# Optimization experiments

Hardware: AMD Instinct MI355X
Metric: run time of the kernel (lower is better)

## Reference

```python
import jax, jax.numpy as jnp
import numpy as np

N, D_IN, H, L, K, Q = 131072, 384, 256, 32, 512, 4


def _lin_init(key, fan_in, fan_out):
    s = 1.0 / np.sqrt(fan_in)
    kw, kb = jax.random.split(key)
    w = jax.random.uniform(kw, (fan_in, fan_out), minval=-s, maxval=s, dtype=jnp.float32)
    b = jax.random.uniform(kb, (fan_out,), minval=-s, maxval=s, dtype=jnp.float32)
    return w, b


def setup_inputs() -> dict:
    key = jax.random.key(0)
    ks = jax.random.split(key, 8)
    enc_w1, enc_b1 = _lin_init(ks[1], D_IN, H)
    enc_w2, enc_b2 = _lin_init(ks[2], H, H)
    enc_w3, enc_b3 = _lin_init(ks[3], H, L)
    dec_w1, dec_b1 = _lin_init(ks[4], L, H)
    dec_w2, dec_b2 = _lin_init(ks[5], H, H)
    dec_w3, dec_b3 = _lin_init(ks[6], H, D_IN)
    codebooks = jax.random.normal(ks[7], (Q, K, L), dtype=jnp.float32) * 0.02
    x = jax.random.normal(ks[0], (N, D_IN), dtype=jnp.float32)
    return dict(x=x,
                enc_w1=enc_w1, enc_b1=enc_b1, enc_w2=enc_w2, enc_b2=enc_b2,
                enc_w3=enc_w3, enc_b3=enc_b3,
                dec_w1=dec_w1, dec_b1=dec_b1, dec_w2=dec_w2, dec_b2=dec_b2,
                dec_w3=dec_w3, dec_b3=dec_b3,
                codebooks=codebooks)


def _encoder(x, w1, b1, w2, b2, w3, b3):
    h = jax.nn.relu(x @ w1 + b1)
    h = jax.nn.relu(h @ w2 + b2)
    return h @ w3 + b3


def _decoder(z, w1, b1, w2, b2, w3, b3):
    h = jax.nn.relu(z @ w1 + b1)
    h = jax.nn.relu(h @ w2 + b2)
    return h @ w3 + b3


def _residual_vq(z, codebooks):
    """Residual VQ: Q stages of nearest-codeword lookup on the running residual.
    Returns (z_quantized with straight-through, indices [N,Q], commitment loss)."""
    residual = z
    quant_sum = jnp.zeros_like(z)
    indices = []
    commit = jnp.float32(0.0)
    for q in range(codebooks.shape[0]):  # small fixed loop over quantizer stages
        cb = codebooks[q]  # [K, L]
        # squared L2 distances [N, K] via expansion (cdist + argmin)
        d = (jnp.sum(residual * residual, axis=-1, keepdims=True)
             - 2.0 * residual @ cb.T
             + jnp.sum(cb * cb, axis=-1))
        idx = jnp.argmin(d, axis=-1)          # [N]
        qv = cb[idx]                          # gather [N, L]
        commit = commit + jnp.mean((jax.lax.stop_gradient(qv) - residual) ** 2)
        quant_sum = quant_sum + qv
        residual = residual - jax.lax.stop_gradient(qv)
        indices.append(idx)
    # straight-through estimator
    z_q = z + jax.lax.stop_gradient(quant_sum - z)
    return z_q, jnp.stack(indices, axis=-1), commit


def reference(x, enc_w1, enc_b1, enc_w2, enc_b2, enc_w3, enc_b3,
              dec_w1, dec_b1, dec_w2, dec_b2, dec_w3, dec_b3, codebooks):
    z = _encoder(x, enc_w1, enc_b1, enc_w2, enc_b2, enc_w3, enc_b3)
    z_q, indices, commit = _residual_vq(z, codebooks)
    x_recon = _decoder(z_q, dec_w1, dec_b1, dec_w2, dec_b2, dec_w3, dec_b3)
    return x_recon, indices, commit
```

## Files before the change

kernel.cpp:

```cpp
#include <hip/hip_runtime.h>
#include <hip/hip_bf16.h>
#include <math.h>


#define N_ROWS 131072
#define D_IN   384
#define H_DIM  256
#define L_DIM  32
#define K_CB   512
#define Q_ST   4
#define VQ_RPB 256
#define NPART  (N_ROWS / VQ_RPB)

typedef __attribute__((ext_vector_type(8))) short short8v;
typedef __attribute__((ext_vector_type(4))) float f32x4;

__device__ __forceinline__ ushort f2bf(float v)
{
    __hip_bfloat16 b = __float2bfloat16(v);
    return *reinterpret_cast<ushort*>(&b);
}

__device__ __forceinline__ float np_sumsq32(const float* __restrict__ v)
{
    #pragma clang fp contract(off)
    float s0 = v[0]*v[0], s1 = v[1]*v[1], s2 = v[2]*v[2], s3 = v[3]*v[3];
    float s4 = v[4]*v[4], s5 = v[5]*v[5], s6 = v[6]*v[6], s7 = v[7]*v[7];
    s0 = s0 + v[8]*v[8];   s1 = s1 + v[9]*v[9];   s2 = s2 + v[10]*v[10]; s3 = s3 + v[11]*v[11];
    s4 = s4 + v[12]*v[12]; s5 = s5 + v[13]*v[13]; s6 = s6 + v[14]*v[14]; s7 = s7 + v[15]*v[15];
    s0 = s0 + v[16]*v[16]; s1 = s1 + v[17]*v[17]; s2 = s2 + v[18]*v[18]; s3 = s3 + v[19]*v[19];
    s4 = s4 + v[20]*v[20]; s5 = s5 + v[21]*v[21]; s6 = s6 + v[22]*v[22]; s7 = s7 + v[23]*v[23];
    s0 = s0 + v[24]*v[24]; s1 = s1 + v[25]*v[25]; s2 = s2 + v[26]*v[26]; s3 = s3 + v[27]*v[27];
    s4 = s4 + v[28]*v[28]; s5 = s5 + v[29]*v[29]; s6 = s6 + v[30]*v[30]; s7 = s7 + v[31]*v[31];
    return ((s0 + s1) + (s2 + s3)) + ((s4 + s5) + (s6 + s7));
}

template<bool RELU>
__global__ __launch_bounds__(256)
void gemm_bias(const float* __restrict__ A, const float* __restrict__ B,
               const float* __restrict__ bias, float* __restrict__ C,
               int K, int Nout)
{
    #pragma clang fp contract(off)
    __shared__ float As2[32][132];
    __shared__ float Bs[32][128];
    const int t  = threadIdx.x;
    const int tc = t & 15;
    const int tr = t >> 4;
    const size_t row0 = (size_t)blockIdx.x * 128;
    const int    col0 = blockIdx.y * 128;

    float acc[8][8];
    #pragma unroll
    for (int i = 0; i < 8; ++i)
        #pragma unroll
        for (int j = 0; j < 8; ++j) acc[i][j] = 0.f;

    const int ar = t >> 3, ak = (t & 7) << 2;
    const int br = t >> 5, bc = (t & 31) << 2;

    for (int k0 = 0; k0 < K; k0 += 32) {
        #pragma unroll
        for (int i = 0; i < 4; ++i) {
            int r = ar + (i << 5);
            float4 v = *reinterpret_cast<const float4*>(A + (row0 + r) * (size_t)K + k0 + ak);
            As2[ak + 0][r] = v.x; As2[ak + 1][r] = v.y;
            As2[ak + 2][r] = v.z; As2[ak + 3][r] = v.w;
        }
        #pragma unroll
        for (int i = 0; i < 4; ++i) {
            int r = br + (i << 3);
            float4 v = *reinterpret_cast<const float4*>(B + (size_t)(k0 + r) * Nout + col0 + bc);
            *reinterpret_cast<float4*>(&Bs[r][bc]) = v;
        }
        __syncthreads();
        #pragma unroll
        for (int k = 0; k < 32; ++k) {
            float a[8], b[8];
            *reinterpret_cast<float4*>(&a[0]) = *reinterpret_cast<const float4*>(&As2[k][tr << 3]);
            *reinterpret_cast<float4*>(&a[4]) = *reinterpret_cast<const float4*>(&As2[k][(tr << 3) + 4]);
            *reinterpret_cast<float4*>(&b[0]) = *reinterpret_cast<const float4*>(&Bs[k][tc << 2]);
            *reinterpret_cast<float4*>(&b[4]) = *reinterpret_cast<const float4*>(&Bs[k][(tc << 2) + 64]);
            #pragma unroll
            for (int i = 0; i < 8; ++i)
                #pragma unroll
                for (int j = 0; j < 8; ++j) acc[i][j] = fmaf(a[i], b[j], acc[i][j]);
        }
        __syncthreads();
    }

    #pragma unroll
    for (int i = 0; i < 8; ++i) {
        size_t r = row0 + (tr << 3) + i;
        int c1 = col0 + (tc << 2);
        int c2 = c1 + 64;
        float v1[4], v2[4];
        #pragma unroll
        for (int j = 0; j < 4; ++j) {
            float u1 = acc[i][j]     + bias[c1 + j];
            float u2 = acc[i][j + 4] + bias[c2 + j];
            if (RELU) { u1 = fmaxf(u1, 0.0f); u2 = fmaxf(u2, 0.0f); }
            v1[j] = u1; v2[j] = u2;
        }
        *reinterpret_cast<float4*>(C + r * Nout + c1) = *reinterpret_cast<float4*>(&v1[0]);
        *reinterpret_cast<float4*>(C + r * Nout + c2) = *reinterpret_cast<float4*>(&v2[0]);
    }
}

__global__ __launch_bounds__(256)
void gemm_z(const float* __restrict__ A, const float* __restrict__ W,
            const float* __restrict__ bv, float* __restrict__ Z)
{
    #pragma clang fp contract(off)
    __shared__ float As2[32][132];
    __shared__ float Ws[32][36];
    const int t = threadIdx.x;
    const int cgz = t & 7, rgz = t >> 3;
    const size_t row0 = (size_t)blockIdx.x * 128;

    float acc[4][4];
    #pragma unroll
    for (int i = 0; i < 4; ++i)
        #pragma unroll
        for (int j = 0; j < 4; ++j) acc[i][j] = 0.f;

    const int ar = t >> 3, ak = (t & 7) << 2;
    for (int k0 = 0; k0 < H_DIM; k0 += 32) {
        #pragma unroll
        for (int i = 0; i < 4; ++i) {
            int r = ar + (i << 5);
            float4 v = *reinterpret_cast<const float4*>(A + (row0 + r) * (size_t)H_DIM + k0 + ak);
            As2[ak + 0][r] = v.x; As2[ak + 1][r] = v.y;
            As2[ak + 2][r] = v.z; As2[ak + 3][r] = v.w;
        }
        {
            int kr = t >> 3, cc = (t & 7) << 2;
            float4 v = *reinterpret_cast<const float4*>(W + (size_t)(k0 + kr) * L_DIM + cc);
            *reinterpret_cast<float4*>(&Ws[kr][cc]) = v;
        }
        __syncthreads();
        #pragma unroll
        for (int k = 0; k < 32; ++k) {
            float a[4], w[4];
            *reinterpret_cast<float4*>(&a[0]) = *reinterpret_cast<const float4*>(&As2[k][rgz << 2]);
            *reinterpret_cast<float4*>(&w[0]) = *reinterpret_cast<const float4*>(&Ws[k][cgz << 2]);
            #pragma unroll
            for (int i = 0; i < 4; ++i)
                #pragma unroll
                for (int j = 0; j < 4; ++j) acc[i][j] = fmaf(a[i], w[j], acc[i][j]);
        }
        __syncthreads();
    }
    #pragma unroll
    for (int i = 0; i < 4; ++i) {
        size_t row = row0 + (rgz << 2) + i;
        float v[4];
        #pragma unroll
        for (int j = 0; j < 4; ++j) v[j] = acc[i][j] + bv[(cgz << 2) + j];
        *reinterpret_cast<float4*>(Z + row * L_DIM + (cgz << 2)) = *reinterpret_cast<float4*>(&v[0]);
    }
}

__global__ __launch_bounds__(256)
void cnorm_kernel(const float* __restrict__ cbs, float* __restrict__ cnorm)
{
    #pragma clang fp contract(off)
    int g = blockIdx.x * 256 + threadIdx.x;
    const float* c = cbs + (size_t)g * L_DIM;
    float cl[L_DIM];
    #pragma unroll
    for (int l = 0; l < L_DIM; ++l) cl[l] = c[l];
    cnorm[g] = np_sumsq32(cl);
}

__global__ __launch_bounds__(256)
void prep_wt(const float* __restrict__ W, ushort* __restrict__ Wt, int K, int N)
{
    int g = blockIdx.x * 256 + threadIdx.x;
    if (g >= K * N) return;
    int n = g / K, k = g - n * K;
    Wt[g] = f2bf(W[(size_t)k * N + n]);
}

__global__ __launch_bounds__(128)
void vq7_kernel(const float* __restrict__ zbuf, const float* __restrict__ cbs,
                const float* __restrict__ cnorm_g, ushort* __restrict__ zqb,
                float* __restrict__ idxOut, double* __restrict__ commitPart,
                int rowBase)
{
    #pragma clang fp contract(off)
    __shared__ float  cbL[K_CB * L_DIM];
    __shared__ float  cnL[K_CB];
    __shared__ double sred[128];

    const int t = threadIdx.x;
    const size_t lrow0 = (size_t)blockIdx.x * VQ_RPB + t;
    const size_t lrow1 = lrow0 + 128;
    const size_t grow0 = (size_t)rowBase + lrow0;
    const size_t grow1 = (size_t)rowBase + lrow1;

    float r0[L_DIM], r1[L_DIM];
    {
        const float4* zp0 = reinterpret_cast<const float4*>(zbuf + lrow0 * L_DIM);
        const float4* zp1 = reinterpret_cast<const float4*>(zbuf + lrow1 * L_DIM);
        #pragma unroll
        for (int j = 0; j < 8; ++j) {
            float4 a = zp0[j], b = zp1[j];
            r0[4*j+0]=a.x; r0[4*j+1]=a.y; r0[4*j+2]=a.z; r0[4*j+3]=a.w;
            r1[4*j+0]=b.x; r1[4*j+1]=b.y; r1[4*j+2]=b.z; r1[4*j+3]=b.w;
        }
    }

    int bidx0[Q_ST], bidx1[Q_ST];
    double cAcc = 0.0;

    #pragma unroll 1
    for (int q = 0; q < Q_ST; ++q) {
        __syncthreads();
        {
            const float4* src = reinterpret_cast<const float4*>(cbs + (size_t)q * K_CB * L_DIM);
            float4* dst = reinterpret_cast<float4*>(cbL);
            #pragma unroll
            for (int i = 0; i < 32; ++i) dst[t + (i << 7)] = src[t + (i << 7)];
            #pragma unroll
            for (int i = 0; i < 4; ++i)
                cnL[t + (i << 7)] = cnorm_g[q * K_CB + t + (i << 7)];
        }
        __syncthreads();

        float rr0 = np_sumsq32(r0);
        float rr1 = np_sumsq32(r1);
        float bd0 = __builtin_inff(), bd1 = __builtin_inff();
        int   bi0 = 0, bi1 = 0;

        #pragma unroll 1
        for (int c = 0; c < K_CB; c += 2) {
            const float4* w0 = reinterpret_cast<const float4*>(cbL + (c << 5));
            const float4* w1 = w0 + 8;
            float a00 = 0.f, a01 = 0.f, a10 = 0.f, a11 = 0.f;
            #pragma unroll
            for (int j = 0; j < 8; ++j) {
                float4 u = w0[j], v = w1[j];
                a00 = fmaf(r0[4*j+0], u.x, a00);  a01 = fmaf(r0[4*j+0], v.x, a01);
                a10 = fmaf(r1[4*j+0], u.x, a10);  a11 = fmaf(r1[4*j+0], v.x, a11);
                a00 = fmaf(r0[4*j+1], u.y, a00);  a01 = fmaf(r0[4*j+1], v.y, a01);
                a10 = fmaf(r1[4*j+1], u.y, a10);  a11 = fmaf(r1[4*j+1], v.y, a11);
                a00 = fmaf(r0[4*j+2], u.z, a00);  a01 = fmaf(r0[4*j+2], v.z, a01);
                a10 = fmaf(r1[4*j+2], u.z, a10);  a11 = fmaf(r1[4*j+2], v.z, a11);
                a00 = fmaf(r0[4*j+3], u.w, a00);  a01 = fmaf(r0[4*j+3], v.w, a01);
                a10 = fmaf(r1[4*j+3], u.w, a10);  a11 = fmaf(r1[4*j+3], v.w, a11);
            }
            float cn0 = cnL[c], cn1 = cnL[c + 1];
            float d00 = (rr0 - 2.0f * a00) + cn0;
            float d01 = (rr0 - 2.0f * a01) + cn1;
            float d10 = (rr1 - 2.0f * a10) + cn0;
            float d11 = (rr1 - 2.0f * a11) + cn1;
            if (d00 < bd0) { bd0 = d00; bi0 = c; }
            if (d01 < bd0) { bd0 = d01; bi0 = c + 1; }
            if (d10 < bd1) { bd1 = d10; bi1 = c; }
            if (d11 < bd1) { bd1 = d11; bi1 = c + 1; }
        }
        bidx0[q] = bi0;
        bidx1[q] = bi1;

        {
            const float4* p0 = reinterpret_cast<const float4*>(cbL + (bi0 << 5));
            const float4* p1 = reinterpret_cast<const float4*>(cbL + (bi1 << 5));
            float cs0 = 0.f, cs1 = 0.f;
            #pragma unroll
            for (int j = 0; j < 8; ++j) {
                float4 v0 = p0[j], v1 = p1[j];
                float df;
                df = v0.x - r0[4*j+0]; cs0 = fmaf(df, df, cs0); r0[4*j+0] = r0[4*j+0] - v0.x;
                df = v0.y - r0[4*j+1]; cs0 = fmaf(df, df, cs0); r0[4*j+1] = r0[4*j+1] - v0.y;
                df = v0.z - r0[4*j+2]; cs0 = fmaf(df, df, cs0); r0[4*j+2] = r0[4*j+2] - v0.z;
                df = v0.w - r0[4*j+3]; cs0 = fmaf(df, df, cs0); r0[4*j+3] = r0[4*j+3] - v0.w;
                df = v1.x - r1[4*j+0]; cs1 = fmaf(df, df, cs1); r1[4*j+0] = r1[4*j+0] - v1.x;
                df = v1.y - r1[4*j+1]; cs1 = fmaf(df, df, cs1); r1[4*j+1] = r1[4*j+1] - v1.y;
                df = v1.z - r1[4*j+2]; cs1 = fmaf(df, df, cs1); r1[4*j+2] = r1[4*j+2] - v1.z;
                df = v1.w - r1[4*j+3]; cs1 = fmaf(df, df, cs1); r1[4*j+3] = r1[4*j+3] - v1.w;
            }
            cAcc += (double)cs0;
            cAcc += (double)cs1;
        }
    }

    {
        float4 iv0 = make_float4((float)bidx0[0], (float)bidx0[1], (float)bidx0[2], (float)bidx0[3]);
        float4 iv1 = make_float4((float)bidx1[0], (float)bidx1[1], (float)bidx1[2], (float)bidx1[3]);
        *reinterpret_cast<float4*>(idxOut + grow0 * Q_ST) = iv0;
        *reinterpret_cast<float4*>(idxOut + grow1 * Q_ST) = iv1;
    }

    {
        const float4* zp0 = reinterpret_cast<const float4*>(zbuf + lrow0 * L_DIM);
        const float4* zp1 = reinterpret_cast<const float4*>(zbuf + lrow1 * L_DIM);
        ushort zq0[L_DIM], zq1[L_DIM];
        #pragma unroll
        for (int j = 0; j < 8; ++j) {
            float4 a = zp0[j], b = zp1[j];
            zq0[4*j+0] = f2bf(a.x - r0[4*j+0]);
            zq0[4*j+1] = f2bf(a.y - r0[4*j+1]);
            zq0[4*j+2] = f2bf(a.z - r0[4*j+2]);
            zq0[4*j+3] = f2bf(a.w - r0[4*j+3]);
            zq1[4*j+0] = f2bf(b.x - r1[4*j+0]);
            zq1[4*j+1] = f2bf(b.y - r1[4*j+1]);
            zq1[4*j+2] = f2bf(b.z - r1[4*j+2]);
            zq1[4*j+3] = f2bf(b.w - r1[4*j+3]);
        }
        uint4* o0 = reinterpret_cast<uint4*>(zqb + lrow0 * L_DIM);
        uint4* o1 = reinterpret_cast<uint4*>(zqb + lrow1 * L_DIM);
        const uint4* s0 = reinterpret_cast<const uint4*>(zq0);
        const uint4* s1 = reinterpret_cast<const uint4*>(zq1);
        #pragma unroll
        for (int j = 0; j < 4; ++j) { o0[j] = s0[j]; o1[j] = s1[j]; }
    }

    sred[t] = cAcc;
    __syncthreads();
    for (int s = 64; s > 0; s >>= 1) {
        if (t < s) sred[t] += sred[t + s];
        __syncthreads();
    }
    if (t == 0) commitPart[rowBase / VQ_RPB + blockIdx.x] = sred[0];
}

template<bool RELU, bool OUTBF16>
__global__ __launch_bounds__(256)
void mfma_gemm(const ushort* __restrict__ A, const ushort* __restrict__ Bt,
               const float* __restrict__ bias, void* __restrict__ Cout,
               int K, int Nout)
{
    __shared__ ushort As[128][40];
    __shared__ ushort Bs[128][40];
    const int t    = threadIdx.x;
    const int lane = t & 63;
    const int wid  = t >> 6;
    const int wr = wid >> 1, wc = wid & 1;
    const size_t row0 = (size_t)blockIdx.x * 128;
    const int    col0 = blockIdx.y * 128;

    f32x4 acc[4][4] = {};
    const int srow = t >> 1;
    const int sh   = (t & 1) << 4;

    for (int k0 = 0; k0 < K; k0 += 32) {
        {
            const ushort* ap = A + (row0 + srow) * (size_t)K + k0 + sh;
            uint4 v0 = *reinterpret_cast<const uint4*>(ap);
            uint4 v1 = *reinterpret_cast<const uint4*>(ap + 8);
            *reinterpret_cast<uint4*>(&As[srow][sh])     = v0;
            *reinterpret_cast<uint4*>(&As[srow][sh + 8]) = v1;
            const ushort* bp = Bt + (size_t)(col0 + srow) * K + k0 + sh;
            uint4 w0 = *reinterpret_cast<const uint4*>(bp);
            uint4 w1 = *reinterpret_cast<const uint4*>(bp + 8);
            *reinterpret_cast<uint4*>(&Bs[srow][sh])     = w0;
            *reinterpret_cast<uint4*>(&Bs[srow][sh + 8]) = w1;
        }
        __syncthreads();
        const int l15 = lane & 15, lk = (lane >> 4) << 3;
        short8v af[4], bf[4];
        #pragma unroll
        for (int f = 0; f < 4; ++f) {
            af[f] = *reinterpret_cast<const short8v*>(&As[(wr << 6) + (f << 4) + l15][lk]);
            bf[f] = *reinterpret_cast<const short8v*>(&Bs[(wc << 6) + (f << 4) + l15][lk]);
        }
        #pragma unroll
        for (int i = 0; i < 4; ++i)
            #pragma unroll
            for (int j = 0; j < 4; ++j)
                acc[i][j] = __builtin_amdgcn_mfma_f32_16x16x32_bf16(af[i], bf[j], acc[i][j], 0, 0, 0);
        __syncthreads();
    }

    const int l15 = lane & 15, lr4 = (lane >> 4) << 2;
    #pragma unroll
    for (int i = 0; i < 4; ++i) {
        #pragma unroll
        for (int j = 0; j < 4; ++j) {
            int col = col0 + (wc << 6) + (j << 4) + l15;
            float bv = bias[col];
            #pragma unroll
            for (int rj = 0; rj < 4; ++rj) {
                size_t row = row0 + (wr << 6) + (i << 4) + lr4 + rj;
                float v = acc[i][j][rj] + bv;
                if (RELU) v = fmaxf(v, 0.f);
                if (OUTBF16)
                    reinterpret_cast<ushort*>(Cout)[row * Nout + col] = f2bf(v);
                else
                    reinterpret_cast<float*>(Cout)[row * Nout + col] = v;
            }
        }
    }
}

__global__ __launch_bounds__(256)
void commit_finalize(const double* __restrict__ commitPart, float* __restrict__ outCommit)
{
    __shared__ double sred[256];
    const int t = threadIdx.x;
    double s = 0.0;
    for (int i = t; i < NPART; i += 256) s += commitPart[i];
    sred[t] = s;
    __syncthreads();
    for (int st = 128; st > 0; st >>= 1) {
        if (t < st) sred[t] += sred[t + st];
        __syncthreads();
    }
    if (t == 0)
        outCommit[0] = (float)(sred[0] / ((double)N_ROWS * (double)L_DIM));
}

extern "C" void kernel_launch(void* const* d_in, const int* in_sizes, int n_in,
                              void* d_out, int out_size, void* d_ws, size_t ws_size,
                              hipStream_t stream)
{
    const float* x      = (const float*)d_in[0];
    const float* enc_w1 = (const float*)d_in[1];
    const float* enc_b1 = (const float*)d_in[2];
    const float* enc_w2 = (const float*)d_in[3];
    const float* enc_b2 = (const float*)d_in[4];
    const float* enc_w3 = (const float*)d_in[5];
    const float* enc_b3 = (const float*)d_in[6];
    const float* dec_w1 = (const float*)d_in[7];
    const float* dec_b1 = (const float*)d_in[8];
    const float* dec_w2 = (const float*)d_in[9];
    const float* dec_b2 = (const float*)d_in[10];
    const float* dec_w3 = (const float*)d_in[11];
    const float* dec_b3 = (const float*)d_in[12];
    const float* cbs    = (const float*)d_in[13];

    float* out       = (float*)d_out;
    float* xrec      = out;
    float* idxOut    = out + (size_t)N_ROWS * D_IN;
    float* commitOut = idxOut + (size_t)N_ROWS * Q_ST;

    char*   wsb        = (char*)d_ws;
    float*  cnorm      = (float*)wsb;
    double* commitPart = (double*)(wsb + 8192);
    ushort* w1t        = (ushort*)(wsb + 12288);
    ushort* w2t        = (ushort*)(wsb + 28672);
    ushort* w3t        = (ushort*)(wsb + 159744);
    char*   bufs       = wsb + 360448;

    size_t availB = (ws_size > 360448) ? ws_size - 360448 : 0;
    long long chunk = (long long)(availB / 3264);
    chunk = (chunk / 256) * 256;
    if (chunk > N_ROWS) chunk = N_ROWS;
    if (chunk < 256) chunk = 256;

    float*  zbuf = (float*)bufs;
    float*  bufA = zbuf + (size_t)chunk * L_DIM;
    float*  bufB = bufA + (size_t)chunk * H_DIM;
    ushort* zqb  = (ushort*)(bufB + (size_t)chunk * H_DIM);
    ushort* h1b  = zqb + (size_t)chunk * L_DIM;
    ushort* h2b  = h1b + (size_t)chunk * H_DIM;

    cnorm_kernel<<<8, 256, 0, stream>>>(cbs, cnorm);
    prep_wt<<<(L_DIM  * H_DIM + 255) / 256, 256, 0, stream>>>(dec_w1, w1t, L_DIM, H_DIM);
    prep_wt<<<(H_DIM * H_DIM + 255) / 256, 256, 0, stream>>>(dec_w2, w2t, H_DIM, H_DIM);
    prep_wt<<<(H_DIM * D_IN + 255) / 256, 256, 0, stream>>>(dec_w3, w3t, H_DIM, D_IN);

    for (long long ro = 0; ro < N_ROWS; ro += chunk) {
        long long R = N_ROWS - ro;
        if (R > chunk) R = chunk;
        dim3 g2((unsigned)(R / 128), 2);
        dim3 g3((unsigned)(R / 128), 3);
        gemm_bias<true><<<g2, 256, 0, stream>>>(x + ro * D_IN, enc_w1, enc_b1, bufA, D_IN, H_DIM);
        gemm_bias<true><<<g2, 256, 0, stream>>>(bufA, enc_w2, enc_b2, bufB, H_DIM, H_DIM);
        gemm_z<<<(unsigned)(R / 128), 256, 0, stream>>>(bufB, enc_w3, enc_b3, zbuf);
        vq7_kernel<<<(unsigned)(R / VQ_RPB), 128, 0, stream>>>(zbuf, cbs, cnorm, zqb,
                                                               idxOut, commitPart, (int)ro);
        mfma_gemm<true,  true ><<<g2, 256, 0, stream>>>(zqb, w1t, dec_b1, h1b, L_DIM, H_DIM);
        mfma_gemm<true,  true ><<<g2, 256, 0, stream>>>(h1b, w2t, dec_b2, h2b, H_DIM, H_DIM);
        mfma_gemm<false, false><<<g3, 256, 0, stream>>>(h2b, w3t, dec_b3, xrec + ro * D_IN, H_DIM, D_IN);
    }

    commit_finalize<<<1, 256, 0, stream>>>(commitPart, commitOut);
}
```

Baseline: 1.068 ms.

## Split VQ codeword search across four waves with shared-memory argmin merge

The VQ kernel now runs 256 threads per block over 128 rows. Each of the four wavefronts scans a quarter of the 512 codewords for the same 64 row pairs, and the per-wave minima are merged through shared memory with lowest-index tie-breaking. This cuts the serial per-thread codeword loop by four and doubles the block count, aiming at better latency hiding and occupancy in the distance search. In exchange it adds an extra barrier and shared-memory merge per stage, repeats the residual update in every wave, and moves the workspace offsets so the larger commit-partial array fits.

New measurement: 932.4 us. 1.15x faster.

```diff
diff --git a/kernel.cpp b/kernel.cpp
--- a/kernel.cpp
+++ b/kernel.cpp
@@ -9,7 +9,7 @@
 #define L_DIM  32
 #define K_CB   512
 #define Q_ST   4
-#define VQ_RPB 256
+#define VQ_RPB 128
 #define NPART  (N_ROWS / VQ_RPB)
 
 typedef __attribute__((ext_vector_type(8))) short short8v;
@@ -182,8 +182,8 @@
     Wt[g] = f2bf(W[(size_t)k * N + n]);
 }
 
-__global__ __launch_bounds__(128)
-void vq7_kernel(const float* __restrict__ zbuf, const float* __restrict__ cbs,
+__global__ __launch_bounds__(256)
+void vq9_kernel(const float* __restrict__ zbuf, const float* __restrict__ cbs,
                 const float* __restrict__ cnorm_g, ushort* __restrict__ zqb,
                 float* __restrict__ idxOut, double* __restrict__ commitPart,
                 int rowBase)
@@ -191,13 +191,18 @@
     #pragma clang fp contract(off)
     __shared__ float  cbL[K_CB * L_DIM];
     __shared__ float  cnL[K_CB];
-    __shared__ double sred[128];
+    __shared__ float  sd0[4][64], sd1[4][64];
+    __shared__ int    si0[4][64], si1[4][64];
+    __shared__ double sred[256];
 
     const int t = threadIdx.x;
-    const size_t lrow0 = (size_t)blockIdx.x * VQ_RPB + t;
-    const size_t lrow1 = lrow0 + 128;
+    const int w = t >> 6;
+    const int l = t & 63;
+    const size_t lrow0 = (size_t)blockIdx.x * VQ_RPB + l;
+    const size_t lrow1 = lrow0 + 64;
     const size_t grow0 = (size_t)rowBase + lrow0;
     const size_t grow1 = (size_t)rowBase + lrow1;
+    const int c0 = w << 7;
 
     float r0[L_DIM], r1[L_DIM];
     {
@@ -221,20 +226,20 @@
             const float4* src = reinterpret_cast<const float4*>(cbs + (size_t)q * K_CB * L_DIM);
             float4* dst = reinterpret_cast<float4*>(cbL);
             #pragma unroll
-            for (int i = 0; i < 32; ++i) dst[t + (i << 7)] = src[t + (i << 7)];
-            #pragma unroll
-            for (int i = 0; i < 4; ++i)
-                cnL[t + (i << 7)] = cnorm_g[q * K_CB + t + (i << 7)];
+            for (int i = 0; i < 16; ++i) dst[t + (i << 8)] = src[t + (i << 8)];
+            cnL[t]       = cnorm_g[q * K_CB + t];
+            cnL[t + 256] = cnorm_g[q * K_CB + t + 256];
         }
         __syncthreads();
 
         float rr0 = np_sumsq32(r0);
         float rr1 = np_sumsq32(r1);
         float bd0 = __builtin_inff(), bd1 = __builtin_inff();
-        int   bi0 = 0, bi1 = 0;
+        int   bi0 = c0, bi1 = c0;
 
         #pragma unroll 1
-        for (int c = 0; c < K_CB; c += 2) {
+        for (int cc = 0; cc < 128; cc += 2) {
+            const int c = c0 + cc;
             const float4* w0 = reinterpret_cast<const float4*>(cbL + (c << 5));
             const float4* w1 = w0 + 8;
             float a00 = 0.f, a01 = 0.f, a10 = 0.f, a11 = 0.f;
@@ -260,12 +265,26 @@
             if (d10 < bd1) { bd1 = d10; bi1 = c; }
             if (d11 < bd1) { bd1 = d11; bi1 = c + 1; }
         }
-        bidx0[q] = bi0;
-        bidx1[q] = bi1;
+
+        sd0[w][l] = bd0; si0[w][l] = bi0;
+        sd1[w][l] = bd1; si1[w][l] = bi1;
+        __syncthreads();
+
+        float g0 = sd0[0][l]; int gi0 = si0[0][l];
+        float g1 = sd1[0][l]; int gi1 = si1[0][l];
+        #pragma unroll
+        for (int ww = 1; ww < 4; ++ww) {
+            float od = sd0[ww][l]; int oi = si0[ww][l];
+            if (od < g0 || (od == g0 && oi < gi0)) { g0 = od; gi0 = oi; }
+            od = sd1[ww][l]; oi = si1[ww][l];
+            if (od < g1 || (od == g1 && oi < gi1)) { g1 = od; gi1 = oi; }
+        }
+        bidx0[q] = gi0;
+        bidx1[q] = gi1;
 
         {
-            const float4* p0 = reinterpret_cast<const float4*>(cbL + (bi0 << 5));
-            const float4* p1 = reinterpret_cast<const float4*>(cbL + (bi1 << 5));
+            const float4* p0 = reinterpret_cast<const float4*>(cbL + (gi0 << 5));
+            const float4* p1 = reinterpret_cast<const float4*>(cbL + (gi1 << 5));
             float cs0 = 0.f, cs1 = 0.f;
             #pragma unroll
             for (int j = 0; j < 8; ++j) {
@@ -280,19 +299,16 @@
                 df = v1.z - r1[4*j+2]; cs1 = fmaf(df, df, cs1); r1[4*j+2] = r1[4*j+2] - v1.z;
                 df = v1.w - r1[4*j+3]; cs1 = fmaf(df, df, cs1); r1[4*j+3] = r1[4*j+3] - v1.w;
             }
-            cAcc += (double)cs0;
-            cAcc += (double)cs1;
-        }
-    }
-
-    {
+            if (w == 0) { cAcc += (double)cs0; cAcc += (double)cs1; }
+        }
+    }
+
+    if (w == 0) {
         float4 iv0 = make_float4((float)bidx0[0], (float)bidx0[1], (float)bidx0[2], (float)bidx0[3]);
         float4 iv1 = make_float4((float)bidx1[0], (float)bidx1[1], (float)bidx1[2], (float)bidx1[3]);
         *reinterpret_cast<float4*>(idxOut + grow0 * Q_ST) = iv0;
         *reinterpret_cast<float4*>(idxOut + grow1 * Q_ST) = iv1;
-    }
-
-    {
+
         const float4* zp0 = reinterpret_cast<const float4*>(zbuf + lrow0 * L_DIM);
         const float4* zp1 = reinterpret_cast<const float4*>(zbuf + lrow1 * L_DIM);
         ushort zq0[L_DIM], zq1[L_DIM];
@@ -316,9 +332,9 @@
         for (int j = 0; j < 4; ++j) { o0[j] = s0[j]; o1[j] = s1[j]; }
     }
 
-    sred[t] = cAcc;
+    sred[t] = (w == 0) ? cAcc : 0.0;
     __syncthreads();
-    for (int s = 64; s > 0; s >>= 1) {
+    for (int s = 128; s > 0; s >>= 1) {
         if (t < s) sred[t] += sred[t + s];
         __syncthreads();
     }
@@ -438,9 +454,9 @@
     char*   wsb        = (char*)d_ws;
     float*  cnorm      = (float*)wsb;
     double* commitPart = (double*)(wsb + 8192);
-    ushort* w1t        = (ushort*)(wsb + 12288);
-    ushort* w2t        = (ushort*)(wsb + 28672);
-    ushort* w3t        = (ushort*)(wsb + 159744);
+    ushort* w1t        = (ushort*)(wsb + 16384);
+    ushort* w2t        = (ushort*)(wsb + 32768);
+    ushort* w3t        = (ushort*)(wsb + 163840);
     char*   bufs       = wsb + 360448;
 
     size_t availB = (ws_size > 360448) ? ws_size - 360448 : 0;
@@ -469,7 +485,7 @@
         gemm_bias<true><<<g2, 256, 0, stream>>>(x + ro * D_IN, enc_w1, enc_b1, bufA, D_IN, H_DIM);
         gemm_bias<true><<<g2, 256, 0, stream>>>(bufA, enc_w2, enc_b2, bufB, H_DIM, H_DIM);
         gemm_z<<<(unsigned)(R / 128), 256, 0, stream>>>(bufB, enc_w3, enc_b3, zbuf);
-        vq7_kernel<<<(unsigned)(R / VQ_RPB), 128, 0, stream>>>(zbuf, cbs, cnorm, zqb,
+        vq9_kernel<<<(unsigned)(R / VQ_RPB), 256, 0, stream>>>(zbuf, cbs, cnorm, zqb,
                                                                idxOut, commitPart, (int)ro);
         mfma_gemm<true,  true ><<<g2, 256, 0, stream>>>(zqb, w1t, dec_b1, h1b, L_DIM, H_DIM);
         mfma_gemm<true,  true ><<<g2, 256, 0, stream>>>(h1b, w2t, dec_b2, h2b, H_DIM, H_DIM);
```
